# Performance work log

Hardware: AMD Instinct MI355X
Metric: run time of the kernel (lower is better)

Reference implementation:

```python
import jax, jax.numpy as jnp
import numpy as np

EPS = 1e-12
W_MAX = 0.8
ALPHA_MAX = 1.5
EXP_CLIP = 20.0
UNARY_TEMP = 1.5
T = 10
ETA = 0.2
ALPHA_SCALE = 1.0

N_NODES = 50000
N_PAIRS = 400000          # undirected pairs; E = 2*N_PAIRS directed edges
IN_DIM = 256
HID = 128
C = 10
EDGE_HID = 64


def setup_inputs() -> dict:
    key = jax.random.key(0)
    ks = jax.random.split(key, 12)
    x = jax.random.normal(ks[0], (N_NODES, IN_DIM), dtype=jnp.float32)
    # symmetric edge list: each undirected pair appears in both directions,
    # rev[e] gives the index of the reversed edge
    src = jax.random.randint(ks[1], (N_PAIRS,), 0, N_NODES, dtype=jnp.int32)
    dst = jax.random.randint(ks[2], (N_PAIRS,), 0, N_NODES, dtype=jnp.int32)
    edge_index = jnp.stack([jnp.concatenate([src, dst]),
                            jnp.concatenate([dst, src])])  # [2, E]
    rev = jnp.concatenate([jnp.arange(N_PAIRS, 2 * N_PAIRS, dtype=jnp.int32),
                           jnp.arange(0, N_PAIRS, dtype=jnp.int32)])
    def lin(k, fan_in, fan_out):
        s = 1.0 / np.sqrt(fan_in)
        return jax.random.uniform(k, (fan_in, fan_out), jnp.float32, -s, s)
    enc_w1 = lin(ks[3], IN_DIM, HID); enc_b1 = jnp.zeros((HID,), jnp.float32)
    enc_w2 = lin(ks[4], HID, C);      enc_b2 = jnp.zeros((C,), jnp.float32)
    em_in = 2 * HID + 2
    em_w1 = lin(ks[5], em_in, EDGE_HID); em_b1 = jnp.zeros((EDGE_HID,), jnp.float32)
    em_w2 = lin(ks[6], EDGE_HID, 1);     em_b2 = jnp.zeros((1,), jnp.float32)
    # xavier_uniform for R_raw
    bound = np.sqrt(6.0 / (C + C))
    R_raw = jax.random.uniform(ks[7], (C, C), jnp.float32, -bound, bound)
    R_scale_log = jnp.asarray(0.0, jnp.float32)
    msg_logit = jnp.asarray(-1.0, jnp.float32)
    return {"x": x, "edge_index": edge_index, "rev": rev,
            "enc_w1": enc_w1, "enc_b1": enc_b1, "enc_w2": enc_w2, "enc_b2": enc_b2,
            "em_w1": em_w1, "em_b1": em_b1, "em_w2": em_w2, "em_b2": em_b2,
            "R_raw": R_raw, "R_scale_log": R_scale_log, "msg_logit": msg_logit}


def reference(x, edge_index, rev, enc_w1, enc_b1, enc_w2, enc_b2,
              em_w1, em_b1, em_w2, em_b2, R_raw, R_scale_log, msg_logit):
    num_nodes = x.shape[0]
    src, dst = edge_index[0], edge_index[1]

    # --- UnaryEncoder (mlp, eval mode: no dropout) ---
    h = jax.nn.relu(x @ enc_w1 + enc_b1)                       # [N, H]
    logits = h @ enc_w2 + enc_b2                               # [N, C]
    log_phi = jax.nn.log_softmax(logits / UNARY_TEMP, axis=-1)

    # --- edge structural features ---
    deg = jax.ops.segment_sum(jnp.ones_like(src, jnp.float32), src,
                              num_segments=num_nodes)           # bincount(src)
    logdeg = jnp.log(deg + 1.0)
    a, b = logdeg[src], logdeg[dst]
    struct = jnp.stack([a + b, jnp.abs(a - b)], axis=-1)        # [E, 2]

    # --- pairwise kernel ---
    hs, hd = h[src], h[dst]
    edge_in = jnp.concatenate([hs * hd, jnp.abs(hs - hd), struct], axis=-1)
    w_raw = (jax.nn.relu(edge_in @ em_w1 + em_b1) @ em_w2 + em_b2)[:, 0]
    w = W_MAX * jax.nn.sigmoid(w_raw)
    w = 0.5 * (w + w[rev])                                      # symmetrize
    R = (jax.nn.softplus(R_scale_log) + 1e-6) * jnp.tanh(0.5 * (R_raw + R_raw.T))
    K = jnp.exp(jnp.clip(w[:, None, None] * R[None], -EXP_CLIP, EXP_CLIP))  # [E,C,C]

    # --- BP ---
    deg_c = jnp.maximum(deg, 1.0)
    edge_norm = (deg_c[src] * deg_c[dst]) ** -0.5               # [E]
    alpha = ALPHA_MAX * jax.nn.sigmoid(msg_logit) * ALPHA_SCALE
    lp_src = log_phi[src]
    m0 = jax.nn.softmax(lp_src, axis=-1)                        # init_unary=True

    def step(m, _):
        f = jnp.einsum('ec,ecd->ed', m, K)
        f = jnp.nan_to_num(f, nan=1.0, posinf=1.0, neginf=1.0)
        log_f = jnp.log(jnp.maximum(f, EPS)) * edge_norm[:, None]
        sum_in = jax.ops.segment_sum(log_f, dst, num_segments=num_nodes)
        excl = sum_in[src] - log_f[rev]
        m_new = jax.nn.softmax(lp_src + alpha * excl, axis=-1)
        m = (1.0 - ETA) * m + ETA * m_new
        m = jnp.maximum(m, EPS)
        m = m / jnp.sum(m, axis=-1, keepdims=True)
        return m, None

    m, _ = jax.lax.scan(step, m0, None, length=T)

    # --- beliefs ---
    f = jnp.einsum('ec,ecd->ed', m, K)
    f = jnp.nan_to_num(f, nan=1.0, posinf=1.0, neginf=1.0)
    log_f = jnp.log(jnp.maximum(f, EPS)) * edge_norm[:, None]
    sum_in = jax.ops.segment_sum(log_f, dst, num_segments=num_nodes)
    beliefs = jax.nn.softmax(log_phi + alpha * sum_in, axis=-1)  # [N, C]
    return beliefs
```

## Files before the change

kernel.cpp:

```cpp
#include <hip/hip_runtime.h>
#include <hip/hip_fp16.h>

#define NN 50000
#define NP 400000
#define NEDGE 800000
#define IND 256
#define HD 128
#define NC 10
#define TBP 10
#define SCAN_NB 196

typedef _Float16 f16;
typedef _Float16 f16x2 __attribute__((ext_vector_type(2)));
typedef _Float16 f16x4 __attribute__((ext_vector_type(4)));
typedef _Float16 f16x8 __attribute__((ext_vector_type(8)));
typedef unsigned short u16x8 __attribute__((ext_vector_type(8)));
typedef float f32x4 __attribute__((ext_vector_type(4)));

static constexpr size_t OFF_R      = 0;
static constexpr size_t OFF_H      = 512;
static constexpr size_t OFF_OFFS   = 512;
static constexpr size_t OFF_CUR    = 512 + 200016;
static constexpr size_t OFF_CSR    = 512 + 400032;
static constexpr size_t OFF_BSUM   = 512 + 3600032;
static constexpr size_t OFF_BBASE  = 512 + 3601056;
static constexpr size_t OFF_LOGPHI = 12800512;
static constexpr size_t OFF_DEG    = 14800512;
static constexpr size_t OFF_LOGDEG = 15000512;
static constexpr size_t OFF_RSQ    = 15200512;
static constexpr size_t OFF_WPAIR  = 15400512;
static constexpr size_t OFF_EN     = 17000512;
static constexpr size_t OFF_M      = 18600512;
static constexpr size_t OFF_L      = 50600512;
static constexpr size_t OFF_SUMIN  = 82600512;
static constexpr size_t OFF_W1T    = 84600512;
static constexpr size_t OFF_W1TE   = 84633280;

__global__ __launch_bounds__(256) void k_setup(const float* __restrict__ Rraw,
    const float* __restrict__ rsl, const float* __restrict__ ml,
    const float* __restrict__ mw1, const float* __restrict__ ew1,
    float* __restrict__ Rbuf, f16* __restrict__ w1t, f16* __restrict__ w1te) {
  int tid = threadIdx.x;
  if (tid < 100) {
    int c = tid / 10, d = tid % 10;
    float scale = log1pf(expf(rsl[0])) + 1e-6f;
    Rbuf[tid] = scale * tanhf(0.5f * (Rraw[c * 10 + d] + Rraw[d * 10 + c]));
  } else if (tid == 100) {
    Rbuf[100] = 1.5f * (1.f / (1.f + expf(-ml[0])));
  }
  for (int idx = tid; idx < 64 * 256; idx += 256) {
    int j = idx >> 8, k = idx & 255;
    w1t[idx] = (f16)mw1[k * 64 + j];
  }
  for (int idx = tid; idx < 128 * 256; idx += 256) {
    int j = idx >> 8, k = idx & 255;
    w1te[idx] = (f16)ew1[k * HD + j];
  }
}

__global__ __launch_bounds__(256) void k_deg(const int* __restrict__ ei, float* __restrict__ deg) {
  int e = blockIdx.x * 256 + threadIdx.x;
  if (e < NEDGE) atomicAdd(&deg[ei[e]], 1.f);
}

__global__ __launch_bounds__(256) void k_nodepost(const float* __restrict__ deg,
    float* __restrict__ logdeg, float* __restrict__ rsq) {
  int i = blockIdx.x * 256 + threadIdx.x;
  if (i >= NN) return;
  float d = deg[i];
  logdeg[i] = __logf(d + 1.f);
  rsq[i] = rsqrtf(fmaxf(d, 1.f));
}

__global__ __launch_bounds__(256) void k_scan1(const float* __restrict__ deg,
    int* __restrict__ bsum) {
  int idx = blockIdx.x * 256 + threadIdx.x;
  int v = (idx < NN) ? (int)deg[idx] : 0;
#pragma unroll
  for (int o = 32; o; o >>= 1) v += __shfl_down(v, o);
  __shared__ int wsum[4];
  if ((threadIdx.x & 63) == 0) wsum[threadIdx.x >> 6] = v;
  __syncthreads();
  if (threadIdx.x == 0) bsum[blockIdx.x] = wsum[0] + wsum[1] + wsum[2] + wsum[3];
}

__global__ __launch_bounds__(256) void k_scan2(const int* __restrict__ bsum,
    int* __restrict__ bbase) {
  __shared__ int s[256];
  int t = threadIdx.x;
  int orig = (t < SCAN_NB) ? bsum[t] : 0;
  s[t] = orig;
  __syncthreads();
  for (int d = 1; d < 256; d <<= 1) {
    int v = (t >= d) ? s[t - d] : 0;
    __syncthreads();
    s[t] += v;
    __syncthreads();
  }
  bbase[t] = s[t] - orig;
}

__global__ __launch_bounds__(256) void k_scan3(const float* __restrict__ deg,
    const int* __restrict__ bbase, int* __restrict__ off, int* __restrict__ cursor) {
  __shared__ int s[256];
  int t = threadIdx.x;
  int idx = blockIdx.x * 256 + t;
  int d = (idx < NN) ? (int)deg[idx] : 0;
  s[t] = d;
  __syncthreads();
  for (int k = 1; k < 256; k <<= 1) {
    int v = (t >= k) ? s[t - k] : 0;
    __syncthreads();
    s[t] += v;
    __syncthreads();
  }
  int base = bbase[blockIdx.x];
  int excl = base + s[t] - d;
  if (idx < NN) {
    off[idx] = excl;
    cursor[idx] = excl;
  }
  if (idx == NN - 1) off[NN] = excl + d;
}

__global__ __launch_bounds__(256) void k_fill(const int* __restrict__ ei,
    int* __restrict__ cursor, int* __restrict__ csr) {
  int e = blockIdx.x * 256 + threadIdx.x;
  if (e >= NEDGE) return;
  int d = ei[NEDGE + e];
  int slot = atomicAdd(&cursor[d], 1);
  csr[slot] = e;
}

__global__ __launch_bounds__(256) void k_encoder(const float* __restrict__ x,
    const f16* __restrict__ w1te, const float* __restrict__ b1, f16* __restrict__ h) {
  __shared__ f16 As[64 * 264];
  const int tid = threadIdx.x;
  const int wid = tid >> 6;
  const int lane = tid & 63;
  const int l15 = lane & 15;
  const int lhi = lane >> 4;
  const int nb = blockIdx.x * 64;
#pragma unroll
  for (int i = 0; i < 16; i++) {
    int fidx = tid + 256 * i;
    int row = fidx >> 6;
    int q = fidx & 63;
    f32x4 v = {0.f, 0.f, 0.f, 0.f};
    if (nb + row < NN) v = *(const f32x4*)(x + (size_t)(nb + row) * IND + q * 4);
    f16x4 o;
#pragma unroll
    for (int j = 0; j < 4; j++) o[j] = (f16)v[j];
    *(f16x4*)(&As[row * 264 + q * 4]) = o;
  }
  __syncthreads();
  f16x8 bfr[8][2];
#pragma unroll
  for (int ks = 0; ks < 8; ks++)
#pragma unroll
    for (int t = 0; t < 2; t++)
      bfr[ks][t] = *(const f16x8*)(w1te + (size_t)(wid * 32 + t * 16 + l15) * 256 + ks * 32 + lhi * 8);
  float b1v[2] = {b1[wid * 32 + l15], b1[wid * 32 + 16 + l15]};
  f32x4 acc[4][2] = {};
#pragma unroll
  for (int ks = 0; ks < 8; ks++) {
    f16x8 af[4];
#pragma unroll
    for (int rt = 0; rt < 4; rt++)
      af[rt] = *(const f16x8*)(&As[(rt * 16 + l15) * 264 + ks * 32 + lhi * 8]);
#pragma unroll
    for (int rt = 0; rt < 4; rt++)
#pragma unroll
      for (int t = 0; t < 2; t++)
        acc[rt][t] = __builtin_amdgcn_mfma_f32_16x16x32_f16(af[rt], bfr[ks][t], acc[rt][t], 0, 0, 0);
  }
#pragma unroll
  for (int rt = 0; rt < 4; rt++) {
#pragma unroll
    for (int t = 0; t < 2; t++) {
#pragma unroll
      for (int i = 0; i < 4; i++) {
        int row = nb + rt * 16 + lhi * 4 + i;
        if (row < NN)
          h[(size_t)row * HD + wid * 32 + t * 16 + l15] = (f16)fmaxf(acc[rt][t][i] + b1v[t], 0.f);
      }
    }
  }
}

__global__ __launch_bounds__(256) void k_logits(const f16* __restrict__ h,
    const float* __restrict__ w2, const float* __restrict__ b2, float* __restrict__ logphi) {
  __shared__ float hs[16 * HD];
  __shared__ float lg[16 * NC];
  const int tid = threadIdx.x;
  const int nb = blockIdx.x * 16;
  for (int i = tid; i < 16 * HD / 8; i += 256) {
    f16x8 v = *(const f16x8*)(h + (size_t)nb * HD + i * 8);
#pragma unroll
    for (int u = 0; u < 8; u++) hs[i * 8 + u] = (float)v[u];
  }
  __syncthreads();
  if (tid < 160) {
    int n = tid / 10, c = tid % 10;
    float a = b2[c];
    for (int k = 0; k < HD; k++) a += hs[n * HD + k] * w2[k * NC + c];
    lg[n * NC + c] = a * (1.f / 1.5f);
  }
  __syncthreads();
  if (tid < 16) {
    float mx = -1e30f;
#pragma unroll
    for (int c = 0; c < NC; c++) mx = fmaxf(mx, lg[tid * NC + c]);
    float s = 0.f;
#pragma unroll
    for (int c = 0; c < NC; c++) s += __expf(lg[tid * NC + c] - mx);
    float lse = __logf(s) + mx;
#pragma unroll
    for (int c = 0; c < NC; c++)
      logphi[(size_t)(nb + tid) * NC + c] = lg[tid * NC + c] - lse;
  }
}

__global__ __launch_bounds__(256) void k_edge_mlp(const f16* __restrict__ h,
    const int* __restrict__ ei, const float* __restrict__ logdeg, const float* __restrict__ rsq,
    const f16* __restrict__ w1t, const float* __restrict__ mw1, const float* __restrict__ mb1,
    const float* __restrict__ mw2, const float* __restrict__ mb2,
    float* __restrict__ w_pair, float* __restrict__ en_pair) {
  __shared__ f16 At[4][16 * 264];
  __shared__ float hidl[4][16 * 64];
  __shared__ float sfeat[4][2][16];
  const int tid = threadIdx.x;
  const int wid = tid >> 6;
  const int lane = tid & 63;
  const int l15 = lane & 15;
  const int lhi = lane >> 4;

  f16x8 bfr[8][4];
#pragma unroll
  for (int ks = 0; ks < 8; ks++)
#pragma unroll
    for (int t = 0; t < 4; t++)
      bfr[ks][t] = *(const f16x8*)(w1t + (size_t)(l15 + 16 * t) * 256 + ks * 32 + lhi * 8);

  float b1v[4], w256v[4], w257v[4];
#pragma unroll
  for (int t = 0; t < 4; t++) {
    b1v[t] = mb1[l15 + 16 * t];
    w256v[t] = mw1[256 * 64 + l15 + 16 * t];
    w257v[t] = mw1[257 * 64 + l15 + 16 * t];
  }
  float w2r[16];
#pragma unroll
  for (int jj = 0; jj < 16; jj++) w2r[jj] = mw2[lhi * 16 + jj];
  const float b2s = mb2[0];

  const int ntiles = NP / 64;
  for (int tile = blockIdx.x; tile < ntiles; tile += gridDim.x) {
    const int pbase = tile * 64 + wid * 16;
#pragma unroll
    for (int rr = 0; rr < 4; rr++) {
      int r = rr * 4 + lhi;
      int p = pbase + r;
      int s = ei[p], d = ei[NEDGE + p];
      f16x8 hv = *(const f16x8*)(h + (size_t)s * HD + l15 * 8);
      f16x8 gv = *(const f16x8*)(h + (size_t)d * HD + l15 * 8);
      f16x8 pv = hv * gv;
      f16x8 qv = hv - gv;
      u16x8 qb = *(u16x8*)&qv;
#pragma unroll
      for (int u = 0; u < 8; u++) qb[u] &= 0x7FFF;
      qv = *(f16x8*)&qb;
      *(f16x8*)(&At[wid][r * 264 + l15 * 8]) = pv;
      *(f16x8*)(&At[wid][r * 264 + 128 + l15 * 8]) = qv;
    }
    if (lane < 16) {
      int p = pbase + lane;
      int s = ei[p], d = ei[NEDGE + p];
      float a = logdeg[s], b = logdeg[d];
      sfeat[wid][0][lane] = a + b;
      sfeat[wid][1][lane] = fabsf(a - b);
      en_pair[p] = rsq[s] * rsq[d];
    }
    __syncthreads();
    f32x4 acc[4] = {{0.f, 0.f, 0.f, 0.f}, {0.f, 0.f, 0.f, 0.f},
                    {0.f, 0.f, 0.f, 0.f}, {0.f, 0.f, 0.f, 0.f}};
#pragma unroll
    for (int ks = 0; ks < 8; ks++) {
      f16x8 af = *(const f16x8*)(&At[wid][l15 * 264 + ks * 32 + lhi * 8]);
#pragma unroll
      for (int t = 0; t < 4; t++)
        acc[t] = __builtin_amdgcn_mfma_f32_16x16x32_f16(af, bfr[ks][t], acc[t], 0, 0, 0);
    }
#pragma unroll
    for (int t = 0; t < 4; t++) {
#pragma unroll
      for (int i = 0; i < 4; i++) {
        int r = lhi * 4 + i;
        float v = acc[t][i] + sfeat[wid][0][r] * w256v[t] + sfeat[wid][1][r] * w257v[t] + b1v[t];
        hidl[wid][r * 64 + l15 + 16 * t] = fmaxf(v, 0.f);
      }
    }
    __syncthreads();
    {
      float sacc = 0.f;
#pragma unroll
      for (int jj = 0; jj < 16; jj++) sacc += hidl[wid][l15 * 64 + lhi * 16 + jj] * w2r[jj];
      sacc += __shfl_xor(sacc, 16);
      sacc += __shfl_xor(sacc, 32);
      if (lane < 16) {
        float wr = sacc + b2s;
        w_pair[pbase + lane] = 0.8f / (1.f + __expf(-wr));
      }
    }
    __syncthreads();
  }
}

__global__ __launch_bounds__(256) void k_m0(const int* __restrict__ ei,
    const float* __restrict__ logphi, f16* __restrict__ m) {
  int e = blockIdx.x * 256 + threadIdx.x;
  if (e >= NEDGE) return;
  int s = ei[e];
  f16x2* mp = (f16x2*)(m + (size_t)e * 10);
  const float2* lp = (const float2*)(logphi + (size_t)s * 10);
#pragma unroll
  for (int i = 0; i < 5; i++) {
    float2 v = lp[i];
    f16x2 o;
    o[0] = (f16)__expf(v.x);
    o[1] = (f16)__expf(v.y);
    mp[i] = o;
  }
}

__global__ __launch_bounds__(256) void k_bp_f(const f16* __restrict__ m,
    const float* __restrict__ wp, const float* __restrict__ enp,
    const float* __restrict__ Rbuf, f16* __restrict__ L) {
  __shared__ float Rs[100];
  if (threadIdx.x < 100) Rs[threadIdx.x] = Rbuf[threadIdx.x];
  __syncthreads();
  int e = blockIdx.x * 256 + threadIdx.x;
  if (e >= NEDGE) return;
  int p = (e < NP) ? e : e - NP;
  float w = wp[p], en = enp[p];
  float mr[10];
  {
    const f16x2* mp = (const f16x2*)(m + (size_t)e * 10);
#pragma unroll
    for (int i = 0; i < 5; i++) { f16x2 v = mp[i]; mr[2 * i] = (float)v[0]; mr[2 * i + 1] = (float)v[1]; }
  }
  float f[10] = {0, 0, 0, 0, 0, 0, 0, 0, 0, 0};
#pragma unroll
  for (int c = 0; c < NC; c++) {
    float Ecc = __expf(w * Rs[c * NC + c]);
    f[c] += mr[c] * Ecc;
#pragma unroll
    for (int d = c + 1; d < NC; d++) {
      float Ecd = __expf(w * Rs[c * NC + d]);
      f[d] += mr[c] * Ecd;
      f[c] += mr[d] * Ecd;
    }
  }
  f16x2* Lp = (f16x2*)(L + (size_t)e * 10);
#pragma unroll
  for (int i = 0; i < 5; i++) {
    f16x2 o;
    o[0] = (f16)(__logf(fmaxf(f[2 * i], 1e-12f)) * en);
    o[1] = (f16)(__logf(fmaxf(f[2 * i + 1], 1e-12f)) * en);
    Lp[i] = o;
  }
}

__global__ __launch_bounds__(256) void k_gather(const f16* __restrict__ L,
    const int* __restrict__ csr, const int* __restrict__ off, float* __restrict__ sumin) {
  int wave = (blockIdx.x * 256 + threadIdx.x) >> 6;
  int lane = threadIdx.x & 63;
  int nl = lane / 10;
  int c = lane % 10;
  int n = wave * 6 + nl;
  if (nl >= 6 || n >= NN) return;
  int o0 = off[n], o1 = off[n + 1];
  float acc = 0.f;
  for (int k = o0; k < o1; k++) {
    int e = csr[k];
    acc += (float)L[(size_t)e * 10 + c];
  }
  sumin[(size_t)n * 10 + c] = acc;
}

__global__ __launch_bounds__(256) void k_bp_fused(f16* __restrict__ m,
    f16* __restrict__ L, const float* __restrict__ sumin,
    const float* __restrict__ logphi, const int* __restrict__ ei,
    const float* __restrict__ wp, const float* __restrict__ enp,
    const float* __restrict__ Rbuf) {
  __shared__ float Rs[104];
  if (threadIdx.x < 101) Rs[threadIdx.x] = Rbuf[threadIdx.x];
  __syncthreads();
  int p = blockIdx.x * 256 + threadIdx.x;
  if (p >= NP) return;
  const float alpha = Rs[100];
  const int s = ei[p], d = ei[NEDGE + p];
  const float w = wp[p], en = enp[p];

  float Le[10], Lr[10];
  {
    const f16x2* a = (const f16x2*)(L + (size_t)p * 10);
    const f16x2* b = (const f16x2*)(L + (size_t)(p + NP) * 10);
#pragma unroll
    for (int i = 0; i < 5; i++) {
      f16x2 u = a[i], v = b[i];
      Le[2 * i] = (float)u[0]; Le[2 * i + 1] = (float)u[1];
      Lr[2 * i] = (float)v[0]; Lr[2 * i + 1] = (float)v[1];
    }
  }
  float te[10], tr[10];
  float mxe = -1e30f, mxr = -1e30f;
  {
    const float2* sis = (const float2*)(sumin + (size_t)s * 10);
    const float2* sid = (const float2*)(sumin + (size_t)d * 10);
    const float2* lps = (const float2*)(logphi + (size_t)s * 10);
    const float2* lpd = (const float2*)(logphi + (size_t)d * 10);
#pragma unroll
    for (int i = 0; i < 5; i++) {
      float2 ss = sis[i], sd = sid[i], ps = lps[i], pd = lpd[i];
      float e0 = ps.x + alpha * (ss.x - Lr[2 * i]);
      float e1 = ps.y + alpha * (ss.y - Lr[2 * i + 1]);
      float r0 = pd.x + alpha * (sd.x - Le[2 * i]);
      float r1 = pd.y + alpha * (sd.y - Le[2 * i + 1]);
      te[2 * i] = e0; te[2 * i + 1] = e1;
      tr[2 * i] = r0; tr[2 * i + 1] = r1;
      mxe = fmaxf(mxe, fmaxf(e0, e1));
      mxr = fmaxf(mxr, fmaxf(r0, r1));
    }
  }
  float se = 0.f, sr = 0.f;
#pragma unroll
  for (int c = 0; c < NC; c++) {
    float ve = __expf(te[c] - mxe);
    float vr = __expf(tr[c] - mxr);
    te[c] = ve; tr[c] = vr;
    se += ve; sr += vr;
  }
  const float ie = 0.2f / se, ir = 0.2f / sr;
  float me[10], mr[10];
  float nse = 0.f, nsr = 0.f;
  {
    f16x2* mpe = (f16x2*)(m + (size_t)p * 10);
    f16x2* mpr = (f16x2*)(m + (size_t)(p + NP) * 10);
#pragma unroll
    for (int i = 0; i < 5; i++) {
      f16x2 u = mpe[i], v = mpr[i];
      float a0 = fmaxf(0.8f * (float)u[0] + te[2 * i] * ie, 1e-12f);
      float a1 = fmaxf(0.8f * (float)u[1] + te[2 * i + 1] * ie, 1e-12f);
      float b0 = fmaxf(0.8f * (float)v[0] + tr[2 * i] * ir, 1e-12f);
      float b1 = fmaxf(0.8f * (float)v[1] + tr[2 * i + 1] * ir, 1e-12f);
      me[2 * i] = a0; me[2 * i + 1] = a1;
      mr[2 * i] = b0; mr[2 * i + 1] = b1;
      nse += a0 + a1; nsr += b0 + b1;
    }
    const float qe = 1.f / nse, qr = 1.f / nsr;
#pragma unroll
    for (int i = 0; i < 5; i++) {
      me[2 * i] *= qe; me[2 * i + 1] *= qe;
      mr[2 * i] *= qr; mr[2 * i + 1] *= qr;
      f16x2 u, v;
      u[0] = (f16)me[2 * i]; u[1] = (f16)me[2 * i + 1];
      v[0] = (f16)mr[2 * i]; v[1] = (f16)mr[2 * i + 1];
      mpe[i] = u; mpr[i] = v;
    }
  }
  float fe[10] = {0, 0, 0, 0, 0, 0, 0, 0, 0, 0};
  float fr[10] = {0, 0, 0, 0, 0, 0, 0, 0, 0, 0};
#pragma unroll
  for (int c = 0; c < NC; c++) {
    float Ecc = __expf(w * Rs[c * NC + c]);
    fe[c] += me[c] * Ecc;
    fr[c] += mr[c] * Ecc;
#pragma unroll
    for (int dd = c + 1; dd < NC; dd++) {
      float E = __expf(w * Rs[c * NC + dd]);
      fe[dd] += me[c] * E; fe[c] += me[dd] * E;
      fr[dd] += mr[c] * E; fr[c] += mr[dd] * E;
    }
  }
  {
    f16x2* Lpe = (f16x2*)(L + (size_t)p * 10);
    f16x2* Lpr = (f16x2*)(L + (size_t)(p + NP) * 10);
#pragma unroll
    for (int i = 0; i < 5; i++) {
      f16x2 u, v;
      u[0] = (f16)(__logf(fmaxf(fe[2 * i], 1e-12f)) * en);
      u[1] = (f16)(__logf(fmaxf(fe[2 * i + 1], 1e-12f)) * en);
      v[0] = (f16)(__logf(fmaxf(fr[2 * i], 1e-12f)) * en);
      v[1] = (f16)(__logf(fmaxf(fr[2 * i + 1], 1e-12f)) * en);
      Lpe[i] = u; Lpr[i] = v;
    }
  }
}

__global__ __launch_bounds__(256) void k_beliefs(const float* __restrict__ logphi,
    const float* __restrict__ sum_in, const float* __restrict__ Rbuf, float* __restrict__ out) {
  int n = blockIdx.x * 256 + threadIdx.x;
  if (n >= NN) return;
  float alpha = Rbuf[100];
  float t[NC];
  float mx = -1e30f;
#pragma unroll
  for (int c = 0; c < NC; c++) {
    float v = logphi[n * NC + c] + alpha * sum_in[n * NC + c];
    t[c] = v;
    mx = fmaxf(mx, v);
  }
  float ssum = 0.f;
#pragma unroll
  for (int c = 0; c < NC; c++) { float ev = __expf(t[c] - mx); t[c] = ev; ssum += ev; }
  float inv = 1.f / ssum;
#pragma unroll
  for (int c = 0; c < NC; c++) out[(size_t)n * NC + c] = t[c] * inv;
}

extern "C" void kernel_launch(void* const* d_in, const int* in_sizes, int n_in,
                              void* d_out, int out_size, void* d_ws, size_t ws_size,
                              hipStream_t stream) {
  const float* x    = (const float*)d_in[0];
  const int*   ei   = (const int*)d_in[1];
  const float* ew1  = (const float*)d_in[3];
  const float* eb1  = (const float*)d_in[4];
  const float* ew2  = (const float*)d_in[5];
  const float* eb2  = (const float*)d_in[6];
  const float* mw1  = (const float*)d_in[7];
  const float* mb1  = (const float*)d_in[8];
  const float* mw2  = (const float*)d_in[9];
  const float* mb2  = (const float*)d_in[10];
  const float* Rraw = (const float*)d_in[11];
  const float* rsl  = (const float*)d_in[12];
  const float* ml   = (const float*)d_in[13];
  float* out = (float*)d_out;

  char* ws = (char*)d_ws;
  float* Rbuf   = (float*)(ws + OFF_R);
  f16*   h      = (f16*)(ws + OFF_H);
  int*   offs   = (int*)(ws + OFF_OFFS);
  int*   cursor = (int*)(ws + OFF_CUR);
  int*   csr    = (int*)(ws + OFF_CSR);
  int*   bsum   = (int*)(ws + OFF_BSUM);
  int*   bbase  = (int*)(ws + OFF_BBASE);
  float* logphi = (float*)(ws + OFF_LOGPHI);
  float* deg    = (float*)(ws + OFF_DEG);
  float* logdeg = (float*)(ws + OFF_LOGDEG);
  float* rsq    = (float*)(ws + OFF_RSQ);
  float* wpair  = (float*)(ws + OFF_WPAIR);
  float* enp    = (float*)(ws + OFF_EN);
  f16*   m      = (f16*)(ws + OFF_M);
  f16*   L      = (f16*)(ws + OFF_L);
  float* sumin  = (float*)(ws + OFF_SUMIN);
  f16*   w1t    = (f16*)(ws + OFF_W1T);
  f16*   w1te   = (f16*)(ws + OFF_W1TE);

  k_setup<<<1, 256, 0, stream>>>(Rraw, rsl, ml, mw1, ew1, Rbuf, w1t, w1te);
  hipMemsetAsync(deg, 0, NN * sizeof(float), stream);
  k_deg<<<NEDGE / 256, 256, 0, stream>>>(ei, deg);
  k_nodepost<<<(NN + 255) / 256, 256, 0, stream>>>(deg, logdeg, rsq);
  k_encoder<<<(NN + 63) / 64, 256, 0, stream>>>(x, w1te, eb1, h);
  k_logits<<<NN / 16, 256, 0, stream>>>(h, ew2, eb2, logphi);
  k_edge_mlp<<<512, 256, 0, stream>>>(h, ei, logdeg, rsq, w1t, mw1, mb1, mw2, mb2, wpair, enp);
  k_scan1<<<SCAN_NB, 256, 0, stream>>>(deg, bsum);
  k_scan2<<<1, 256, 0, stream>>>(bsum, bbase);
  k_scan3<<<SCAN_NB, 256, 0, stream>>>(deg, bbase, offs, cursor);
  k_fill<<<NEDGE / 256, 256, 0, stream>>>(ei, cursor, csr);
  k_m0<<<NEDGE / 256, 256, 0, stream>>>(ei, logphi, m);
  k_bp_f<<<NEDGE / 256, 256, 0, stream>>>(m, wpair, enp, Rbuf, L);

  const int gblocks = (NN + 23) / 24;
  const int fblocks = (NP + 255) / 256;
  for (int it = 0; it < TBP; it++) {
    k_gather<<<gblocks, 256, 0, stream>>>(L, csr, offs, sumin);
    k_bp_fused<<<fblocks, 256, 0, stream>>>(m, L, sumin, logphi, ei, wpair, enp, Rbuf);
  }
  k_gather<<<gblocks, 256, 0, stream>>>(L, csr, offs, sumin);
  k_beliefs<<<(NN + 255) / 256, 256, 0, stream>>>(logphi, sumin, Rbuf, out);
}
```

Baseline: 990.9 us.

## Fuse BP iterations into a persistent cooperative kernel with grid syncs

Replaces the 22 per-iteration launches of gather and edge-update kernels with one cooperative persistent kernel that loops over the iterations, using grid.sync between the gather and edge phases. Each thread keeps its pair's edge data, messages and log-factors in registers across iterations, so the message array is no longer read back and written to global memory. In exchange, occupancy is capped by a heavy register footprint (4 edge slots × 20 f16x2 arrays) and each grid-wide barrier adds latency. The gather is also spread over a fixed number of waves with a static node partition, which may balance work worse than the old layout. The old multi-kernel path remains as a fallback if the cooperative launch is not possible.

```diff
diff --git a/kernel.cpp b/kernel.cpp
--- a/kernel.cpp
+++ b/kernel.cpp
@@ -1,5 +1,8 @@
 #include <hip/hip_runtime.h>
 #include <hip/hip_fp16.h>
+#include <hip/hip_cooperative_groups.h>
+
+namespace cg = cooperative_groups;
 
 #define NN 50000
 #define NP 400000
@@ -9,6 +12,7 @@
 #define NC 10
 #define TBP 10
 #define SCAN_NB 196
+#define NCU 256
 
 typedef _Float16 f16;
 typedef _Float16 f16x2 __attribute__((ext_vector_type(2)));
@@ -494,6 +498,186 @@
       v[0] = (f16)(__logf(fmaxf(fr[2 * i], 1e-12f)) * en);
       v[1] = (f16)(__logf(fmaxf(fr[2 * i + 1], 1e-12f)) * en);
       Lpe[i] = u; Lpr[i] = v;
+    }
+  }
+}
+
+__global__ __launch_bounds__(256, 2) void k_coop(
+    const int* __restrict__ ei, const float* __restrict__ wp, const float* __restrict__ enp,
+    const float* __restrict__ logphi, const float* __restrict__ Rbuf,
+    f16* __restrict__ L, float* __restrict__ sumin,
+    const int* __restrict__ csr, const int* __restrict__ offs) {
+  cg::grid_group grid = cg::this_grid();
+  __shared__ float Rs[104];
+  if (threadIdx.x < 101) Rs[threadIdx.x] = Rbuf[threadIdx.x];
+  __syncthreads();
+  const float alpha = Rs[100];
+  const int T = (int)gridDim.x * 256;
+  const int tid = blockIdx.x * 256 + threadIdx.x;
+  const int lane = threadIdx.x & 63;
+  const int gwave = tid >> 6;
+  const int waves = T >> 6;
+  const int npw = (NN + waves - 1) / waves;
+  const int nl = lane / 10;
+  const int ch = lane % 10;
+
+  int sA[4], dA[4];
+  float wA[4], enA[4];
+  f16x2 mP[4][10];
+  f16x2 lP[4][10];
+
+#pragma unroll
+  for (int sl = 0; sl < 4; sl++) {
+    int p = tid + sl * T;
+    if (p >= NP) { sA[sl] = -1; continue; }
+    int sn = ei[p], dn = ei[NEDGE + p];
+    float w = wp[p], en = enp[p];
+    sA[sl] = sn; dA[sl] = dn; wA[sl] = w; enA[sl] = en;
+    float me[10], mr[10];
+    {
+      const float2* lps = (const float2*)(logphi + (size_t)sn * 10);
+      const float2* lpd = (const float2*)(logphi + (size_t)dn * 10);
+#pragma unroll
+      for (int i = 0; i < 5; i++) {
+        float2 a = lps[i], b = lpd[i];
+        f16x2 u, v;
+        u[0] = (f16)__expf(a.x); u[1] = (f16)__expf(a.y);
+        v[0] = (f16)__expf(b.x); v[1] = (f16)__expf(b.y);
+        mP[sl][i] = u; mP[sl][5 + i] = v;
+        me[2 * i] = (float)u[0]; me[2 * i + 1] = (float)u[1];
+        mr[2 * i] = (float)v[0]; mr[2 * i + 1] = (float)v[1];
+      }
+    }
+    float fe[10] = {0, 0, 0, 0, 0, 0, 0, 0, 0, 0};
+    float fr[10] = {0, 0, 0, 0, 0, 0, 0, 0, 0, 0};
+#pragma unroll
+    for (int c = 0; c < NC; c++) {
+      float Ecc = __expf(w * Rs[c * NC + c]);
+      fe[c] += me[c] * Ecc;
+      fr[c] += mr[c] * Ecc;
+#pragma unroll
+      for (int dd = c + 1; dd < NC; dd++) {
+        float E = __expf(w * Rs[c * NC + dd]);
+        fe[dd] += me[c] * E; fe[c] += me[dd] * E;
+        fr[dd] += mr[c] * E; fr[c] += mr[dd] * E;
+      }
+    }
+    f16x2* Lpe = (f16x2*)(L + (size_t)p * 10);
+    f16x2* Lpr = (f16x2*)(L + (size_t)(p + NP) * 10);
+#pragma unroll
+    for (int i = 0; i < 5; i++) {
+      f16x2 u, v;
+      u[0] = (f16)(__logf(fmaxf(fe[2 * i], 1e-12f)) * en);
+      u[1] = (f16)(__logf(fmaxf(fe[2 * i + 1], 1e-12f)) * en);
+      v[0] = (f16)(__logf(fmaxf(fr[2 * i], 1e-12f)) * en);
+      v[1] = (f16)(__logf(fmaxf(fr[2 * i + 1], 1e-12f)) * en);
+      lP[sl][i] = u; lP[sl][5 + i] = v;
+      Lpe[i] = u; Lpr[i] = v;
+    }
+  }
+
+  for (int it = 0; it <= TBP; it++) {
+    grid.sync();
+    if (nl < 6) {
+      int nb = gwave * npw;
+      for (int n0 = 0; n0 < npw; n0 += 6) {
+        int n = nb + n0 + nl;
+        if (n < nb + npw && n < NN) {
+          int o0 = offs[n], o1 = offs[n + 1];
+          float acc = 0.f;
+          for (int k = o0; k < o1; k++)
+            acc += (float)L[(size_t)csr[k] * 10 + ch];
+          sumin[(size_t)n * 10 + ch] = acc;
+        }
+      }
+    }
+    if (it == TBP) break;
+    grid.sync();
+#pragma unroll
+    for (int sl = 0; sl < 4; sl++) {
+      if (sA[sl] < 0) continue;
+      const int p = tid + sl * T;
+      const int sn = sA[sl], dn = dA[sl];
+      const float w = wA[sl], en = enA[sl];
+      float te[10], tr[10];
+      float mxe = -1e30f, mxr = -1e30f;
+      {
+        const float2* sis = (const float2*)(sumin + (size_t)sn * 10);
+        const float2* sid = (const float2*)(sumin + (size_t)dn * 10);
+        const float2* lps = (const float2*)(logphi + (size_t)sn * 10);
+        const float2* lpd = (const float2*)(logphi + (size_t)dn * 10);
+#pragma unroll
+        for (int i = 0; i < 5; i++) {
+          float2 ss = sis[i], sd = sid[i], ps = lps[i], pd = lpd[i];
+          f16x2 lu = lP[sl][i], lv = lP[sl][5 + i];
+          float e0 = ps.x + alpha * (ss.x - (float)lv[0]);
+          float e1 = ps.y + alpha * (ss.y - (float)lv[1]);
+          float r0 = pd.x + alpha * (sd.x - (float)lu[0]);
+          float r1 = pd.y + alpha * (sd.y - (float)lu[1]);
+          te[2 * i] = e0; te[2 * i + 1] = e1;
+          tr[2 * i] = r0; tr[2 * i + 1] = r1;
+          mxe = fmaxf(mxe, fmaxf(e0, e1));
+          mxr = fmaxf(mxr, fmaxf(r0, r1));
+        }
+      }
+      float se = 0.f, sr = 0.f;
+#pragma unroll
+      for (int c = 0; c < NC; c++) {
+        float ve = __expf(te[c] - mxe);
+        float vr = __expf(tr[c] - mxr);
+        te[c] = ve; tr[c] = vr;
+        se += ve; sr += vr;
+      }
+      const float ie = 0.2f / se, ir = 0.2f / sr;
+      float me[10], mr[10];
+      float nse = 0.f, nsr = 0.f;
+#pragma unroll
+      for (int i = 0; i < 5; i++) {
+        f16x2 u = mP[sl][i], v = mP[sl][5 + i];
+        float a0 = fmaxf(0.8f * (float)u[0] + te[2 * i] * ie, 1e-12f);
+        float a1 = fmaxf(0.8f * (float)u[1] + te[2 * i + 1] * ie, 1e-12f);
+        float b0 = fmaxf(0.8f * (float)v[0] + tr[2 * i] * ir, 1e-12f);
+        float b1 = fmaxf(0.8f * (float)v[1] + tr[2 * i + 1] * ir, 1e-12f);
+        me[2 * i] = a0; me[2 * i + 1] = a1;
+        mr[2 * i] = b0; mr[2 * i + 1] = b1;
+        nse += a0 + a1; nsr += b0 + b1;
+      }
+      const float qe = 1.f / nse, qr = 1.f / nsr;
+#pragma unroll
+      for (int i = 0; i < 5; i++) {
+        me[2 * i] *= qe; me[2 * i + 1] *= qe;
+        mr[2 * i] *= qr; mr[2 * i + 1] *= qr;
+        f16x2 u, v;
+        u[0] = (f16)me[2 * i]; u[1] = (f16)me[2 * i + 1];
+        v[0] = (f16)mr[2 * i]; v[1] = (f16)mr[2 * i + 1];
+        mP[sl][i] = u; mP[sl][5 + i] = v;
+      }
+      float fe[10] = {0, 0, 0, 0, 0, 0, 0, 0, 0, 0};
+      float fr[10] = {0, 0, 0, 0, 0, 0, 0, 0, 0, 0};
+#pragma unroll
+      for (int c = 0; c < NC; c++) {
+        float Ecc = __expf(w * Rs[c * NC + c]);
+        fe[c] += me[c] * Ecc;
+        fr[c] += mr[c] * Ecc;
+#pragma unroll
+        for (int dd = c + 1; dd < NC; dd++) {
+          float E = __expf(w * Rs[c * NC + dd]);
+          fe[dd] += me[c] * E; fe[c] += me[dd] * E;
+          fr[dd] += mr[c] * E; fr[c] += mr[dd] * E;
+        }
+      }
+      f16x2* Lpe = (f16x2*)(L + (size_t)p * 10);
+      f16x2* Lpr = (f16x2*)(L + (size_t)(p + NP) * 10);
+#pragma unroll
+      for (int i = 0; i < 5; i++) {
+        f16x2 u, v;
+        u[0] = (f16)(__logf(fmaxf(fe[2 * i], 1e-12f)) * en);
+        u[1] = (f16)(__logf(fmaxf(fe[2 * i + 1], 1e-12f)) * en);
+        v[0] = (f16)(__logf(fmaxf(fr[2 * i], 1e-12f)) * en);
+        v[1] = (f16)(__logf(fmaxf(fr[2 * i + 1], 1e-12f)) * en);
+        lP[sl][i] = u; lP[sl][5 + i] = v;
+        Lpe[i] = u; Lpr[i] = v;
+      }
     }
   }
 }
@@ -568,15 +752,28 @@
   k_scan2<<<1, 256, 0, stream>>>(bsum, bbase);
   k_scan3<<<SCAN_NB, 256, 0, stream>>>(deg, bbase, offs, cursor);
   k_fill<<<NEDGE / 256, 256, 0, stream>>>(ei, cursor, csr);
-  k_m0<<<NEDGE / 256, 256, 0, stream>>>(ei, logphi, m);
-  k_bp_f<<<NEDGE / 256, 256, 0, stream>>>(m, wpair, enp, Rbuf, L);
-
-  const int gblocks = (NN + 23) / 24;
-  const int fblocks = (NP + 255) / 256;
-  for (int it = 0; it < TBP; it++) {
+
+  int maxblk = 0;
+  hipError_t qerr = hipOccupancyMaxActiveBlocksPerMultiprocessor(&maxblk, k_coop, 256, 0);
+  bool coop = (qerr == hipSuccess) && (maxblk >= 2);
+  if (coop) {
+    int nblk = (maxblk >= 4 ? 4 : maxblk) * NCU;
+    void* args[] = {(void*)&ei, (void*)&wpair, (void*)&enp, (void*)&logphi,
+                    (void*)&Rbuf, (void*)&L, (void*)&sumin, (void*)&csr, (void*)&offs};
+    hipError_t lerr = hipLaunchCooperativeKernel((void*)k_coop, dim3(nblk), dim3(256),
+                                                 args, 0, stream);
+    if (lerr != hipSuccess) coop = false;
+  }
+  if (!coop) {
+    k_m0<<<NEDGE / 256, 256, 0, stream>>>(ei, logphi, m);
+    k_bp_f<<<NEDGE / 256, 256, 0, stream>>>(m, wpair, enp, Rbuf, L);
+    const int gblocks = (NN + 23) / 24;
+    const int fblocks = (NP + 255) / 256;
+    for (int it = 0; it < TBP; it++) {
+      k_gather<<<gblocks, 256, 0, stream>>>(L, csr, offs, sumin);
+      k_bp_fused<<<fblocks, 256, 0, stream>>>(m, L, sumin, logphi, ei, wpair, enp, Rbuf);
+    }
     k_gather<<<gblocks, 256, 0, stream>>>(L, csr, offs, sumin);
-    k_bp_fused<<<fblocks, 256, 0, stream>>>(m, L, sumin, logphi, ei, wpair, enp, Rbuf);
-  }
-  k_gather<<<gblocks, 256, 0, stream>>>(L, csr, offs, sumin);
+  }
   k_beliefs<<<(NN + 255) / 256, 256, 0, stream>>>(logphi, sumin, Rbuf, out);
 }
```

New measurement: 988.8 us. No clear change (-0.2%).
